# Optimization experiments

Measured on AMD Instinct MI355X. Metric: run time of the kernel, lower is better.

Reference implementation:

```python
import jax, jax.numpy as jnp
import numpy as np

B, T, D, H, L = 64, 512, 1024, 1024, 2


def _make_params(key, in_size, hidden):
    # 4 input-to-hidden and 4 hidden-to-hidden matrices, gate order (i, f, n, o),
    # concatenated along the output axis -> one GEMM per source per step.
    k1, k2 = jax.random.split(key)
    sx = (6.0 / (in_size + hidden)) ** 0.5   # xavier_uniform bound
    sh = (6.0 / (hidden + hidden)) ** 0.5
    Wx = jax.random.uniform(k1, (in_size, 4 * hidden), minval=-sx, maxval=sx, dtype=jnp.float32)
    Wh = jax.random.uniform(k2, (hidden, 4 * hidden), minval=-sh, maxval=sh, dtype=jnp.float32)
    b = jnp.zeros((4 * hidden,), dtype=jnp.float32)
    return Wx, Wh, b


def setup_inputs() -> dict:
    key = jax.random.key(0)
    kx, k0, k1 = jax.random.split(key, 3)
    x = jax.random.normal(kx, (B, T, D), dtype=jnp.float32)
    h0 = jnp.zeros((L, B, H), dtype=jnp.float32)
    c0 = jnp.zeros((L, B, H), dtype=jnp.float32)
    Wx0, Wh0, b0 = _make_params(k0, D, H)
    Wx1, Wh1, b1 = _make_params(k1, H, H)
    return {"x": x, "h0": h0, "c0": c0,
            "Wx0": Wx0, "Wh0": Wh0, "b0": b0,
            "Wx1": Wx1, "Wh1": Wh1, "b1": b1}


def _run_layer(xseq, h, c, Wx, Wh, b):
    # xseq: [T, B, in], h/c: [B, H]
    def step(carry, xt):
        h, c = carry
        g = xt @ Wx + h @ Wh + b                       # [B, 4H]
        i_t, f_t, n_t, o_t = jnp.split(g, 4, axis=-1)
        i_t = jax.nn.sigmoid(i_t)
        f_t = jax.nn.sigmoid(f_t)
        n_t = jnp.tanh(n_t)
        o_t = jax.nn.sigmoid(o_t)
        c = f_t * c + i_t * n_t
        h = o_t * jnp.tanh(c)
        return (h, c), h
    (h, c), ys = jax.lax.scan(step, (h, c), xseq)
    return ys, h, c                                     # ys: [T, B, H]


def reference(x, h0, c0, Wx0, Wh0, b0, Wx1, Wh1, b1):
    xs = jnp.transpose(x, (1, 0, 2))                    # [T, B, D]
    params = [(Wx0, Wh0, b0), (Wx1, Wh1, b1)]
    hs, cs = [], []
    for layer in range(L):
        Wx, Wh, b = params[layer]
        xs, h, c = _run_layer(xs, h0[layer], c0[layer], Wx, Wh, b)
        hs.append(h)
        cs.append(c)
    outputs = jnp.transpose(xs, (1, 0, 2))              # [B, T, H]
    return outputs, (jnp.stack(hs, 0), jnp.stack(cs, 0))
```

## Files before the change

kernel.cpp:

```cpp
#include <hip/hip_runtime.h>


#define NBLK 256
#define TPB  512
#define T_   512
#define HS_OFF 33554432
#define CS_OFF 33685504

typedef float  f32x4  __attribute__((ext_vector_type(4)));
typedef short  bf16x8 __attribute__((ext_vector_type(8)));

#define WS_CTR  0u
#define WS_W    139264u
#define WS_BIAS 33693696u
#define WS_XB   33726464u
#define WS_H0   100835328u
#define WS_H1   101097472u
#define WS_MIN  101359616u

__device__ __forceinline__ unsigned short f2bf(float f) {
  union { float f; unsigned u; } v; v.f = f;
  return (unsigned short)((v.u + 0x7FFFu + ((v.u >> 16) & 1u)) >> 16);
}
__device__ __forceinline__ float fsig(float x) { return 1.0f / (1.0f + __expf(-x)); }
__device__ __forceinline__ float ftanh(float x) {
  x = fminf(15.0f, fmaxf(-15.0f, x));
  float e = __expf(2.0f * x);
  return (e - 1.0f) / (e + 1.0f);
}

__global__ void kw(const float* __restrict__ Wx0, const float* __restrict__ Wh0,
                   const float* __restrict__ Wx1, const float* __restrict__ Wh1,
                   unsigned short* __restrict__ wp) {
  __shared__ float tile[64][65];
  int tb = blockIdx.x;
  int m  = tb >> 10;
  int kt = (tb >> 6) & 15;
  int nt = tb & 63;
  const float* W = (m == 0) ? Wx0 : (m == 1) ? Wh0 : (m == 2) ? Wx1 : Wh1;
  unsigned short* O = wp + (size_t)m * 4194304u;
  int k0 = kt * 64, n0 = nt * 64;
  int tx = threadIdx.x & 63, tg = threadIdx.x >> 6;
  for (int r = tg; r < 64; r += 4)
    tile[r][tx] = W[(size_t)(k0 + r) * 4096 + n0 + tx];
  __syncthreads();
  for (int r = tg; r < 64; r += 4) {
    int n = n0 + r;
    int p = ((n & 1023) << 2) | (n >> 10);
    O[(size_t)p * 1024 + k0 + tx] = f2bf(tile[tx][r]);
  }
}

__global__ void kx(const float* __restrict__ x, unsigned short* __restrict__ xb) {
  int row = blockIdx.x;
  int t = row >> 6, b = row & 63;
  const float4* src = (const float4*)(x + ((size_t)b * 512 + t) * 1024);
  float4 f = src[threadIdx.x];
  ushort4 o; o.x = f2bf(f.x); o.y = f2bf(f.y); o.z = f2bf(f.z); o.w = f2bf(f.w);
  ((ushort4*)(xb + (size_t)row * 1024))[threadIdx.x] = o;
}

__global__ void kmisc(const float* __restrict__ b0, const float* __restrict__ b1,
                      const float* __restrict__ h0in,
                      float* __restrict__ biasP,
                      unsigned short* __restrict__ h0r, unsigned short* __restrict__ h1r) {
  int idx = blockIdx.x * 256 + threadIdx.x;
  if (idx < 8192) {
    int layer = idx >> 12, p = idx & 4095;
    int orig = (p & 3) * 1024 + (p >> 2);
    biasP[idx] = (layer ? b1 : b0)[orig];
  } else if (idx < 139264) {
    int e = idx - 8192;
    int layer = e >> 16, o = e & 65535;
    int row = o >> 10, col = o & 1023;
    unsigned short v = f2bf(h0in[layer * 65536 + o]);
    int dst = 65536 + (col >> 3) * 512 + row * 8 + (col & 7);
    if (layer) h1r[dst] = v; else h0r[dst] = v;
  }
}

__global__ void __launch_bounds__(TPB, 2)
klstm(const float* __restrict__ c0_in,
      const unsigned short* __restrict__ wp,
      const float* __restrict__ biasP,
      const unsigned short* __restrict__ xb,
      unsigned short* __restrict__ h0ring,
      unsigned short* __restrict__ h1ring,
      unsigned* __restrict__ ctrbase,
      float* __restrict__ out) {
  extern __shared__ char smem[];
  float* red  = (float*)(smem + 131072);
  float* lhb  = (float*)(smem + 139264);
  float* xred = (float*)(smem + 141312);
  unsigned* gctr  = ctrbase;
  unsigned* rctr  = ctrbase + 16384;
  unsigned* gflag = ctrbase + 17408;
  const int tid = threadIdx.x;
  const int w   = tid >> 6;
  const int l   = tid & 63;
  const int bid = blockIdx.x;
  const int n0  = bid * 16;
  const int layer = w >> 2;
  const int rbase = (w & 3) * 16;
  const int khalf = (w >> 2) * 512;
  const int grp   = bid >> 4;
  float* lh = lhb + w * 64;

  {
    const int msrc[4] = {0, 2, 1, 3};
    for (int s = 0; s < 4; ++s) {
      const char* src = (const char*)(wp + (size_t)msrc[s] * 4194304u + (size_t)n0 * 1024u);
      char* dst = smem + s * 32768;
      for (int i = tid; i < 2048; i += TPB) {
        int kreg = i & 3, col = (i >> 2) & 15, kkf = i >> 6;
        int srcb = col * 2048 + (kkf >> 4) * 1024 + (kkf & 15) * 64 + kreg * 16;
        *(uint4*)(dst + i * 16) = *(const uint4*)(src + srcb);
      }
    }
  }

  const int jg = bid * 4 + ((l & 15) >> 2);
  const float biasv = biasP[layer * 4096 + n0 + (l & 15)];
  const int qb = l & ~3;

  float cr[4];
  #pragma unroll
  for (int v = 0; v < 4; ++v)
    cr[v] = c0_in[layer * 65536 + (rbase + (l >> 4) * 4 + v) * 1024 + jg];

  const int ae0  = (rbase + (l & 15)) * 1024 + khalf + (l >> 4) * 8;
  const int hbase = ((khalf >> 3) + (l >> 4)) * 512 + (rbase + (l & 15)) * 8;
  const int kqb   = (w >> 2) * 16384;
  const int bfrag = ((l & 15) * 4 + (l >> 4)) * 16;
  const int hsto = (bid >> 1) * 512 + 4 * (bid & 1);

  __syncthreads();

  f32x4 xacc = {0.f, 0.f, 0.f, 0.f};
  {
    #pragma unroll
    for (int kk = 0; kk < 16; ++kk) {
      bf16x8 ax = *(const bf16x8*)(xb + ae0 + kk * 32);
      bf16x8 b  = *(const bf16x8*)(smem + kqb + kk * 1024 + bfrag);
      xacc = __builtin_amdgcn_mfma_f32_16x16x32_bf16(ax, b, xacc, 0, 0, 0);
    }
    if (w >= 4) {
      float* xr = xred + (size_t)(w & 3) * 256 + (size_t)l * 4;
      #pragma unroll
      for (int v = 0; v < 4; ++v) xr[v] = xacc[v];
    }
  }
  __syncthreads();

  for (int k = 0; k <= T_; ++k) {
    const unsigned short* h0p = h0ring + ((k + 1) & 1) * 65536;
    const unsigned short* h1p = h1ring + (k & 1) * 65536;

    bf16x8 hf0[16], hf1[16];
    #pragma unroll
    for (int kk = 0; kk < 16; ++kk) {
      hf0[kk] = *(const bf16x8*)(h0p + hbase + kk * 2048);
      hf1[kk] = *(const bf16x8*)(h1p + hbase + kk * 2048);
    }

    f32x4 acc0  = {0.f, 0.f, 0.f, 0.f};
    f32x4 acc1a = {0.f, 0.f, 0.f, 0.f};
    f32x4 acc1b = {0.f, 0.f, 0.f, 0.f};
    #pragma unroll
    for (int kk = 0; kk < 16; ++kk) {
      const int bo = kqb + kk * 1024 + bfrag;
      bf16x8 bh0 = *(const bf16x8*)(smem + 65536 + bo);
      bf16x8 bx1 = *(const bf16x8*)(smem + 32768 + bo);
      bf16x8 bh1 = *(const bf16x8*)(smem + 98304 + bo);
      acc0  = __builtin_amdgcn_mfma_f32_16x16x32_bf16(hf0[kk], bh0, acc0, 0, 0, 0);
      acc1a = __builtin_amdgcn_mfma_f32_16x16x32_bf16(hf0[kk], bx1, acc1a, 0, 0, 0);
      acc1b = __builtin_amdgcn_mfma_f32_16x16x32_bf16(hf1[kk], bh1, acc1b, 0, 0, 0);
    }

    {
      float* rb = red + (size_t)(w * 64 + l) * 4;
      f32x4 other = layer ? acc0 : (acc1a + acc1b);
      #pragma unroll
      for (int v = 0; v < 4; ++v) rb[v] = other[v];
    }
    __syncthreads();

    f32x4 g = layer ? (acc1a + acc1b) : acc0;
    {
      const int pw = layer ? (w - 4) : (w + 4);
      const float* rb = red + (size_t)(pw * 64 + l) * 4;
      #pragma unroll
      for (int v = 0; v < 4; ++v) g[v] += rb[v];
    }
    if (w < 4) {
      const float* xr = xred + (size_t)w * 256 + (size_t)l * 4;
      #pragma unroll
      for (int v = 0; v < 4; ++v) g[v] += xacc[v] + xr[v];
    }

    const bool active = layer ? (k >= 1) : (k < T_);
    f32x4 outv = {0.f, 0.f, 0.f, 0.f};
    if (active) {
      unsigned short* hw = layer ? (h1ring + ((k + 1) & 1) * 65536)
                                 : (h0ring + (k & 1) * 65536);
      #pragma unroll
      for (int v = 0; v < 4; ++v) {
        float gv = g[v] + biasv;
        float gi = __shfl(gv, qb);
        float gf = __shfl(gv, qb | 1);
        float gn = __shfl(gv, qb | 2);
        float go = __shfl(gv, qb | 3);
        float i_ = fsig(gi), f_ = fsig(gf), n_ = ftanh(gn), o_ = fsig(go);
        float c = f_ * cr[v] + i_ * n_;
        cr[v] = c;
        float h = o_ * ftanh(c);
        if ((l & 3) == 0)
          lh[((l >> 4) * 4 + v) * 4 + ((l & 15) >> 2)] = h;
      }
      if (l < 16) {
        f32x4 h4 = *(f32x4*)(lh + l * 4);
        outv = h4;
        ushort4 u4;
        u4.x = f2bf(h4[0]); u4.y = f2bf(h4[1]); u4.z = f2bf(h4[2]); u4.w = f2bf(h4[3]);
        union { ushort4 s; unsigned long long q; } pk; pk.s = u4;
        __hip_atomic_store((unsigned long long*)(hw + hsto + (rbase + l) * 8), pk.q,
                           __ATOMIC_RELAXED, __HIP_MEMORY_SCOPE_AGENT);
      }
    }

    if (k < T_) {
      __syncthreads();
      if (tid == 0) {
        unsigned old = __hip_atomic_fetch_add(&gctr[grp * 1024 + k], 1u,
                                              __ATOMIC_RELAXED, __HIP_MEMORY_SCOPE_AGENT);
        if (old == 15u) {
          unsigned oldr = __hip_atomic_fetch_add(&rctr[k], 1u,
                                                 __ATOMIC_RELAXED, __HIP_MEMORY_SCOPE_AGENT);
          if (oldr == 15u) {
            #pragma unroll
            for (int gg = 0; gg < 16; ++gg)
              __hip_atomic_store(&gflag[gg * 1024 + k], 1u,
                                 __ATOMIC_RELAXED, __HIP_MEMORY_SCOPE_AGENT);
          }
        }
        __builtin_amdgcn_fence(__ATOMIC_ACQUIRE, "agent");
      }
    }

    if (active && l < 16) {
      const int row = rbase + l;
      if (layer) {
        *(f32x4*)(out + (size_t)row * 524288u + (size_t)(k - 1) * 1024u + bid * 4) = outv;
        if (k == T_)
          *(f32x4*)(out + HS_OFF + 65536 + row * 1024 + bid * 4) = outv;
      } else if (k == T_ - 1) {
        *(f32x4*)(out + HS_OFF + row * 1024 + bid * 4) = outv;
      }
    }
    if (k + 1 < T_) {
      const unsigned short* xt = xb + (size_t)(k + 1) * 65536u;
      f32x4 xa = {0.f, 0.f, 0.f, 0.f};
      #pragma unroll
      for (int kk = 0; kk < 16; ++kk) {
        bf16x8 ax = *(const bf16x8*)(xt + ae0 + kk * 32);
        bf16x8 b  = *(const bf16x8*)(smem + kqb + kk * 1024 + bfrag);
        xa = __builtin_amdgcn_mfma_f32_16x16x32_bf16(ax, b, xa, 0, 0, 0);
      }
      if (w >= 4) {
        float* xr = xred + (size_t)(w & 3) * 256 + (size_t)l * 4;
        #pragma unroll
        for (int v = 0; v < 4; ++v) xr[v] = xa[v];
      } else {
        xacc = xa;
      }
    }

    if (k < T_) {
      if (tid == 0) {
        unsigned spins = 0;
        while (__hip_atomic_load(&gflag[grp * 1024 + k], __ATOMIC_RELAXED, __HIP_MEMORY_SCOPE_AGENT) == 0u) {
          __builtin_amdgcn_s_sleep(1);
          if (++spins > 67108864u) break;
        }
      }
      __syncthreads();
    }
  }

  if ((l & 3) == 0) {
    #pragma unroll
    for (int v = 0; v < 4; ++v)
      out[CS_OFF + layer * 65536 + (rbase + (l >> 4) * 4 + v) * 1024 + jg] = cr[v];
  }
}

extern "C" void kernel_launch(void* const* d_in, const int* in_sizes, int n_in,
                              void* d_out, int out_size, void* d_ws, size_t ws_size,
                              hipStream_t stream) {
  const float* x   = (const float*)d_in[0];
  const float* h0  = (const float*)d_in[1];
  const float* c0  = (const float*)d_in[2];
  const float* Wx0 = (const float*)d_in[3];
  const float* Wh0 = (const float*)d_in[4];
  const float* b0  = (const float*)d_in[5];
  const float* Wx1 = (const float*)d_in[6];
  const float* Wh1 = (const float*)d_in[7];
  const float* b1  = (const float*)d_in[8];
  float* out = (float*)d_out;
  char* ws = (char*)d_ws;
  if (ws_size < (size_t)WS_MIN) return;

  unsigned* ctr       = (unsigned*)(ws + WS_CTR);
  unsigned short* wp  = (unsigned short*)(ws + WS_W);
  float* biasP        = (float*)(ws + WS_BIAS);
  unsigned short* xbp = (unsigned short*)(ws + WS_XB);
  unsigned short* h0r = (unsigned short*)(ws + WS_H0);
  unsigned short* h1r = (unsigned short*)(ws + WS_H1);

  (void)hipMemsetAsync(ctr, 0, 139264, stream);
  hipLaunchKernelGGL(kw,    dim3(4096),  dim3(256), 0, stream, Wx0, Wh0, Wx1, Wh1, wp);
  hipLaunchKernelGGL(kx,    dim3(32768), dim3(256), 0, stream, x, xbp);
  hipLaunchKernelGGL(kmisc, dim3(544),   dim3(256), 0, stream, b0, b1, h0, biasP, h0r, h1r);

  (void)hipFuncSetAttribute((const void*)klstm, hipFuncAttributeMaxDynamicSharedMemorySize, 145408);
  const float* c0a = c0; const unsigned short* wpa = wp; const float* bpa = biasP;
  const unsigned short* xba = xbp;
  unsigned short* h0a = h0r; unsigned short* h1a = h1r;
  unsigned* ca = ctr; float* oa = out;
  void* args[] = {&c0a, &wpa, &bpa, &xba, &h0a, &h1a, &ca, &oa};
  hipError_t e = hipLaunchCooperativeKernel((const void*)klstm, dim3(NBLK), dim3(TPB),
                                            args, 145408, stream);
  if (e != hipSuccess) {
    hipLaunchKernelGGL(klstm, dim3(NBLK), dim3(TPB), 145408, stream,
                       c0a, wpa, bpa, xba, h0a, h1a, ca, oa);
  }
}
```

Before: 5.425 ms.

## Split layers across block halves with decoupled per-layer barriers and ring buffer

Each of the 256 blocks previously computed a 16-column slice for both layers, which required an intra-block reduction and a single grid-wide barrier per step. Now blocks 0-127 handle layer 0 and blocks 128-255 handle layer 1, each block owning 32 columns with the full K range. Each layer gets its own grid counters and flags, and the layer-0 hidden state goes into an 8-deep ring so layer 0 can run up to 8 steps ahead of layer 1. The intent is to drop the cross-wave LDS reduction and let the two layers pipeline instead of running in lockstep, at the cost of more spin-wait logic and per-block work that may not balance, since layer-1 blocks perform two recurrent GEMMs per step.

```diff
diff --git a/kernel.cpp b/kernel.cpp
--- a/kernel.cpp
+++ b/kernel.cpp
@@ -11,12 +11,12 @@
 typedef short  bf16x8 __attribute__((ext_vector_type(8)));
 
 #define WS_CTR  0u
-#define WS_W    139264u
-#define WS_BIAS 33693696u
-#define WS_XB   33726464u
-#define WS_H0   100835328u
-#define WS_H1   101097472u
-#define WS_MIN  101359616u
+#define WS_W    40960u
+#define WS_BIAS 33595392u
+#define WS_XB   33628160u
+#define WS_H0   100737024u
+#define WS_H1   101785600u
+#define WS_MIN  102047744u
 
 __device__ __forceinline__ unsigned short f2bf(float f) {
   union { float f; unsigned u; } v; v.f = f;
@@ -74,8 +74,9 @@
     int layer = e >> 16, o = e & 65535;
     int row = o >> 10, col = o & 1023;
     unsigned short v = f2bf(h0in[layer * 65536 + o]);
-    int dst = 65536 + (col >> 3) * 512 + row * 8 + (col & 7);
-    if (layer) h1r[dst] = v; else h0r[dst] = v;
+    int ds = (col >> 3) * 512 + row * 8 + (col & 7);
+    if (layer) h1r[65536 + ds] = v;
+    else       h0r[7 * 65536 + ds] = v;
   }
 }
 
@@ -89,120 +90,132 @@
       unsigned* __restrict__ ctrbase,
       float* __restrict__ out) {
   extern __shared__ char smem[];
-  float* red  = (float*)(smem + 131072);
-  float* lhb  = (float*)(smem + 139264);
-  float* xred = (float*)(smem + 141312);
-  unsigned* gctr  = ctrbase;
-  unsigned* rctr  = ctrbase + 16384;
-  unsigned* gflag = ctrbase + 17408;
+  float* lhb = (float*)(smem + 131072);
+  unsigned* gctr0 = ctrbase;
+  unsigned* rctr0 = ctrbase + 4096;
+  unsigned* flag0 = ctrbase + 4608;
+  unsigned* gctr1 = ctrbase + 5120;
+  unsigned* rctr1 = ctrbase + 9216;
+  unsigned* flag1 = ctrbase + 9728;
   const int tid = threadIdx.x;
   const int w   = tid >> 6;
   const int l   = tid & 63;
   const int bid = blockIdx.x;
-  const int n0  = bid * 16;
-  const int layer = w >> 2;
+  const int isL1 = bid >> 7;
+  const int b    = bid & 127;
+  const int cg   = w >> 2;
   const int rbase = (w & 3) * 16;
-  const int khalf = (w >> 2) * 512;
-  const int grp   = bid >> 4;
+  const int n0   = b * 32;
+  const int grp  = b >> 4;
   float* lh = lhb + w * 64;
 
   {
-    const int msrc[4] = {0, 2, 1, 3};
-    for (int s = 0; s < 4; ++s) {
-      const char* src = (const char*)(wp + (size_t)msrc[s] * 4194304u + (size_t)n0 * 1024u);
-      char* dst = smem + s * 32768;
-      for (int i = tid; i < 2048; i += TPB) {
-        int kreg = i & 3, col = (i >> 2) & 15, kkf = i >> 6;
-        int srcb = col * 2048 + (kkf >> 4) * 1024 + (kkf & 15) * 64 + kreg * 16;
+    const int mA = isL1 ? 3 : 1;
+    const int mB = isL1 ? 2 : 0;
+    for (int s = 0; s < 2; ++s) {
+      int m = s ? mB : mA;
+      const char* src = (const char*)(wp + (size_t)m * 4194304u + (size_t)n0 * 1024u);
+      char* dst = smem + s * 65536;
+      for (int i = tid; i < 4096; i += TPB) {
+        int kreg = i & 3, col = (i >> 2) & 15, kk = (i >> 6) & 31, cgg = i >> 11;
+        int srcb = (cgg * 16 + col) * 2048 + kk * 64 + kreg * 16;
         *(uint4*)(dst + i * 16) = *(const uint4*)(src + srcb);
       }
     }
   }
 
-  const int jg = bid * 4 + ((l & 15) >> 2);
-  const float biasv = biasP[layer * 4096 + n0 + (l & 15)];
+  const float biasv = biasP[isL1 * 4096 + n0 + cg * 16 + (l & 15)];
   const int qb = l & ~3;
+  const int jg = b * 8 + cg * 4 + ((l & 15) >> 2);
 
   float cr[4];
   #pragma unroll
   for (int v = 0; v < 4; ++v)
-    cr[v] = c0_in[layer * 65536 + (rbase + (l >> 4) * 4 + v) * 1024 + jg];
-
-  const int ae0  = (rbase + (l & 15)) * 1024 + khalf + (l >> 4) * 8;
-  const int hbase = ((khalf >> 3) + (l >> 4)) * 512 + (rbase + (l & 15)) * 8;
-  const int kqb   = (w >> 2) * 16384;
+    cr[v] = c0_in[isL1 * 65536 + (rbase + (l >> 4) * 4 + v) * 1024 + jg];
+
+  const int hfb   = (l >> 4) * 512 + (rbase + (l & 15)) * 8;
   const int bfrag = ((l & 15) * 4 + (l >> 4)) * 16;
-  const int hsto = (bid >> 1) * 512 + 4 * (bid & 1);
+  const int ae0   = (rbase + (l & 15)) * 1024 + (l >> 4) * 8;
+  const int bslot0 = cg * 32768;
+  const int bslot1 = 65536 + cg * 32768;
+  const int hsto  = b * 512 + cg * 4;
 
   __syncthreads();
 
   f32x4 xacc = {0.f, 0.f, 0.f, 0.f};
-  {
+  if (!isL1) {
     #pragma unroll
-    for (int kk = 0; kk < 16; ++kk) {
+    for (int kk = 0; kk < 32; ++kk) {
       bf16x8 ax = *(const bf16x8*)(xb + ae0 + kk * 32);
-      bf16x8 b  = *(const bf16x8*)(smem + kqb + kk * 1024 + bfrag);
-      xacc = __builtin_amdgcn_mfma_f32_16x16x32_bf16(ax, b, xacc, 0, 0, 0);
-    }
-    if (w >= 4) {
-      float* xr = xred + (size_t)(w & 3) * 256 + (size_t)l * 4;
-      #pragma unroll
-      for (int v = 0; v < 4; ++v) xr[v] = xacc[v];
-    }
-  }
-  __syncthreads();
-
-  for (int k = 0; k <= T_; ++k) {
-    const unsigned short* h0p = h0ring + ((k + 1) & 1) * 65536;
-    const unsigned short* h1p = h1ring + (k & 1) * 65536;
-
-    bf16x8 hf0[16], hf1[16];
-    #pragma unroll
-    for (int kk = 0; kk < 16; ++kk) {
-      hf0[kk] = *(const bf16x8*)(h0p + hbase + kk * 2048);
-      hf1[kk] = *(const bf16x8*)(h1p + hbase + kk * 2048);
-    }
-
-    f32x4 acc0  = {0.f, 0.f, 0.f, 0.f};
-    f32x4 acc1a = {0.f, 0.f, 0.f, 0.f};
-    f32x4 acc1b = {0.f, 0.f, 0.f, 0.f};
-    #pragma unroll
-    for (int kk = 0; kk < 16; ++kk) {
-      const int bo = kqb + kk * 1024 + bfrag;
-      bf16x8 bh0 = *(const bf16x8*)(smem + 65536 + bo);
-      bf16x8 bx1 = *(const bf16x8*)(smem + 32768 + bo);
-      bf16x8 bh1 = *(const bf16x8*)(smem + 98304 + bo);
-      acc0  = __builtin_amdgcn_mfma_f32_16x16x32_bf16(hf0[kk], bh0, acc0, 0, 0, 0);
-      acc1a = __builtin_amdgcn_mfma_f32_16x16x32_bf16(hf0[kk], bx1, acc1a, 0, 0, 0);
-      acc1b = __builtin_amdgcn_mfma_f32_16x16x32_bf16(hf1[kk], bh1, acc1b, 0, 0, 0);
-    }
-
+      bf16x8 bx = *(const bf16x8*)(smem + bslot1 + kk * 1024 + bfrag);
+      xacc = __builtin_amdgcn_mfma_f32_16x16x32_bf16(ax, bx, xacc, 0, 0, 0);
+    }
+  }
+
+  for (int k = 0; k < T_; ++k) {
+    if (tid == 0) {
+      unsigned spins = 0;
+      if (!isL1) {
+        if (k > 0)
+          while (__hip_atomic_load(&flag0[k - 1], __ATOMIC_RELAXED, __HIP_MEMORY_SCOPE_AGENT) == 0u)
+            { __builtin_amdgcn_s_sleep(1); if (++spins > 67108864u) break; }
+        if (k >= 8)
+          while (__hip_atomic_load(&flag1[k - 8], __ATOMIC_RELAXED, __HIP_MEMORY_SCOPE_AGENT) == 0u)
+            { __builtin_amdgcn_s_sleep(1); if (++spins > 67108864u) break; }
+      } else {
+        if (k > 0)
+          while (__hip_atomic_load(&flag1[k - 1], __ATOMIC_RELAXED, __HIP_MEMORY_SCOPE_AGENT) == 0u)
+            { __builtin_amdgcn_s_sleep(1); if (++spins > 67108864u) break; }
+        while (__hip_atomic_load(&flag0[k], __ATOMIC_RELAXED, __HIP_MEMORY_SCOPE_AGENT) == 0u)
+          { __builtin_amdgcn_s_sleep(1); if (++spins > 67108864u) break; }
+      }
+    }
+    __syncthreads();
+
+    f32x4 a0 = {0.f,0.f,0.f,0.f}, a1 = {0.f,0.f,0.f,0.f};
+    f32x4 a2 = {0.f,0.f,0.f,0.f}, a3 = {0.f,0.f,0.f,0.f};
+    if (!isL1) {
+      const unsigned short* hp = h0ring + (size_t)((k + 7) & 7) * 65536;
+      bf16x8 hf[32];
+      #pragma unroll
+      for (int kk = 0; kk < 32; ++kk) hf[kk] = *(const bf16x8*)(hp + hfb + kk * 2048);
+      #pragma unroll
+      for (int kk = 0; kk < 32; kk += 2) {
+        a0 = __builtin_amdgcn_mfma_f32_16x16x32_bf16(hf[kk],
+               *(const bf16x8*)(smem + bslot0 + kk * 1024 + bfrag), a0, 0, 0, 0);
+        a1 = __builtin_amdgcn_mfma_f32_16x16x32_bf16(hf[kk + 1],
+               *(const bf16x8*)(smem + bslot0 + (kk + 1) * 1024 + bfrag), a1, 0, 0, 0);
+      }
+    } else {
+      const unsigned short* hp0 = h0ring + (size_t)(k & 7) * 65536;
+      const unsigned short* hp1 = h1ring + (size_t)((k + 1) & 1) * 65536;
+      #pragma unroll
+      for (int kk = 0; kk < 32; kk += 2) {
+        bf16x8 f0a = *(const bf16x8*)(hp0 + hfb + kk * 2048);
+        bf16x8 f1a = *(const bf16x8*)(hp1 + hfb + kk * 2048);
+        bf16x8 f0b = *(const bf16x8*)(hp0 + hfb + (kk + 1) * 2048);
+        bf16x8 f1b = *(const bf16x8*)(hp1 + hfb + (kk + 1) * 2048);
+        a0 = __builtin_amdgcn_mfma_f32_16x16x32_bf16(f1a,
+               *(const bf16x8*)(smem + bslot0 + kk * 1024 + bfrag), a0, 0, 0, 0);
+        a2 = __builtin_amdgcn_mfma_f32_16x16x32_bf16(f0a,
+               *(const bf16x8*)(smem + bslot1 + kk * 1024 + bfrag), a2, 0, 0, 0);
+        a1 = __builtin_amdgcn_mfma_f32_16x16x32_bf16(f1b,
+               *(const bf16x8*)(smem + bslot0 + (kk + 1) * 1024 + bfrag), a1, 0, 0, 0);
+        a3 = __builtin_amdgcn_mfma_f32_16x16x32_bf16(f0b,
+               *(const bf16x8*)(smem + bslot1 + (kk + 1) * 1024 + bfrag), a3, 0, 0, 0);
+      }
+    }
+
+    f32x4 g = (a0 + a1) + (a2 + a3);
+    if (!isL1) {
+      #pragma unroll
+      for (int v = 0; v < 4; ++v) g[v] += xacc[v];
+    }
+
+    f32x4 outv = {0.f, 0.f, 0.f, 0.f};
     {
-      float* rb = red + (size_t)(w * 64 + l) * 4;
-      f32x4 other = layer ? acc0 : (acc1a + acc1b);
-      #pragma unroll
-      for (int v = 0; v < 4; ++v) rb[v] = other[v];
-    }
-    __syncthreads();
-
-    f32x4 g = layer ? (acc1a + acc1b) : acc0;
-    {
-      const int pw = layer ? (w - 4) : (w + 4);
-      const float* rb = red + (size_t)(pw * 64 + l) * 4;
-      #pragma unroll
-      for (int v = 0; v < 4; ++v) g[v] += rb[v];
-    }
-    if (w < 4) {
-      const float* xr = xred + (size_t)w * 256 + (size_t)l * 4;
-      #pragma unroll
-      for (int v = 0; v < 4; ++v) g[v] += xacc[v] + xr[v];
-    }
-
-    const bool active = layer ? (k >= 1) : (k < T_);
-    f32x4 outv = {0.f, 0.f, 0.f, 0.f};
-    if (active) {
-      unsigned short* hw = layer ? (h1ring + ((k + 1) & 1) * 65536)
-                                 : (h0ring + (k & 1) * 65536);
+      unsigned short* hw = isL1 ? (h1ring + (size_t)(k & 1) * 65536)
+                                : (h0ring + (size_t)(k & 7) * 65536);
       #pragma unroll
       for (int v = 0; v < 4; ++v) {
         float gv = g[v] + biasv;
@@ -228,69 +241,48 @@
       }
     }
 
-    if (k < T_) {
-      __syncthreads();
-      if (tid == 0) {
-        unsigned old = __hip_atomic_fetch_add(&gctr[grp * 1024 + k], 1u,
-                                              __ATOMIC_RELAXED, __HIP_MEMORY_SCOPE_AGENT);
-        if (old == 15u) {
-          unsigned oldr = __hip_atomic_fetch_add(&rctr[k], 1u,
-                                                 __ATOMIC_RELAXED, __HIP_MEMORY_SCOPE_AGENT);
-          if (oldr == 15u) {
-            #pragma unroll
-            for (int gg = 0; gg < 16; ++gg)
-              __hip_atomic_store(&gflag[gg * 1024 + k], 1u,
-                                 __ATOMIC_RELAXED, __HIP_MEMORY_SCOPE_AGENT);
-          }
+    __syncthreads();
+    if (tid == 0) {
+      unsigned* gc = (isL1 ? gctr1 : gctr0) + grp * 512 + k;
+      unsigned old = __hip_atomic_fetch_add(gc, 1u, __ATOMIC_RELAXED, __HIP_MEMORY_SCOPE_AGENT);
+      if (old == 15u) {
+        unsigned* rc = (isL1 ? rctr1 : rctr0) + k;
+        unsigned oldr = __hip_atomic_fetch_add(rc, 1u, __ATOMIC_RELAXED, __HIP_MEMORY_SCOPE_AGENT);
+        if (oldr == 7u)
+          __hip_atomic_store(&(isL1 ? flag1 : flag0)[k], 1u,
+                             __ATOMIC_RELAXED, __HIP_MEMORY_SCOPE_AGENT);
+      }
+      __builtin_amdgcn_fence(__ATOMIC_ACQUIRE, "agent");
+    }
+
+    if (isL1) {
+      if (l < 16) {
+        const int row = rbase + l;
+        *(f32x4*)(out + (size_t)row * 524288u + (size_t)k * 1024u + b * 8 + cg * 4) = outv;
+        if (k == T_ - 1)
+          *(f32x4*)(out + HS_OFF + 65536 + row * 1024 + b * 8 + cg * 4) = outv;
+      }
+    } else {
+      if (k == T_ - 1 && l < 16)
+        *(f32x4*)(out + HS_OFF + (rbase + l) * 1024 + b * 8 + cg * 4) = outv;
+      if (k + 1 < T_) {
+        const unsigned short* xt = xb + (size_t)(k + 1) * 65536u;
+        f32x4 xa = {0.f, 0.f, 0.f, 0.f};
+        #pragma unroll
+        for (int kk = 0; kk < 32; ++kk) {
+          bf16x8 ax = *(const bf16x8*)(xt + ae0 + kk * 32);
+          bf16x8 bx = *(const bf16x8*)(smem + bslot1 + kk * 1024 + bfrag);
+          xa = __builtin_amdgcn_mfma_f32_16x16x32_bf16(ax, bx, xa, 0, 0, 0);
         }
-        __builtin_amdgcn_fence(__ATOMIC_ACQUIRE, "agent");
-      }
-    }
-
-    if (active && l < 16) {
-      const int row = rbase + l;
-      if (layer) {
-        *(f32x4*)(out + (size_t)row * 524288u + (size_t)(k - 1) * 1024u + bid * 4) = outv;
-        if (k == T_)
-          *(f32x4*)(out + HS_OFF + 65536 + row * 1024 + bid * 4) = outv;
-      } else if (k == T_ - 1) {
-        *(f32x4*)(out + HS_OFF + row * 1024 + bid * 4) = outv;
-      }
-    }
-    if (k + 1 < T_) {
-      const unsigned short* xt = xb + (size_t)(k + 1) * 65536u;
-      f32x4 xa = {0.f, 0.f, 0.f, 0.f};
-      #pragma unroll
-      for (int kk = 0; kk < 16; ++kk) {
-        bf16x8 ax = *(const bf16x8*)(xt + ae0 + kk * 32);
-        bf16x8 b  = *(const bf16x8*)(smem + kqb + kk * 1024 + bfrag);
-        xa = __builtin_amdgcn_mfma_f32_16x16x32_bf16(ax, b, xa, 0, 0, 0);
-      }
-      if (w >= 4) {
-        float* xr = xred + (size_t)(w & 3) * 256 + (size_t)l * 4;
-        #pragma unroll
-        for (int v = 0; v < 4; ++v) xr[v] = xa[v];
-      } else {
         xacc = xa;
       }
-    }
-
-    if (k < T_) {
-      if (tid == 0) {
-        unsigned spins = 0;
-        while (__hip_atomic_load(&gflag[grp * 1024 + k], __ATOMIC_RELAXED, __HIP_MEMORY_SCOPE_AGENT) == 0u) {
-          __builtin_amdgcn_s_sleep(1);
-          if (++spins > 67108864u) break;
-        }
-      }
-      __syncthreads();
     }
   }
 
   if ((l & 3) == 0) {
     #pragma unroll
     for (int v = 0; v < 4; ++v)
-      out[CS_OFF + layer * 65536 + (rbase + (l >> 4) * 4 + v) * 1024 + jg] = cr[v];
+      out[CS_OFF + isL1 * 65536 + (rbase + (l >> 4) * 4 + v) * 1024 + jg] = cr[v];
   }
 }
 
@@ -317,21 +309,21 @@
   unsigned short* h0r = (unsigned short*)(ws + WS_H0);
   unsigned short* h1r = (unsigned short*)(ws + WS_H1);
 
-  (void)hipMemsetAsync(ctr, 0, 139264, stream);
+  (void)hipMemsetAsync(ctr, 0, 40960, stream);
   hipLaunchKernelGGL(kw,    dim3(4096),  dim3(256), 0, stream, Wx0, Wh0, Wx1, Wh1, wp);
   hipLaunchKernelGGL(kx,    dim3(32768), dim3(256), 0, stream, x, xbp);
   hipLaunchKernelGGL(kmisc, dim3(544),   dim3(256), 0, stream, b0, b1, h0, biasP, h0r, h1r);
 
-  (void)hipFuncSetAttribute((const void*)klstm, hipFuncAttributeMaxDynamicSharedMemorySize, 145408);
+  (void)hipFuncSetAttribute((const void*)klstm, hipFuncAttributeMaxDynamicSharedMemorySize, 133120);
   const float* c0a = c0; const unsigned short* wpa = wp; const float* bpa = biasP;
   const unsigned short* xba = xbp;
   unsigned short* h0a = h0r; unsigned short* h1a = h1r;
   unsigned* ca = ctr; float* oa = out;
   void* args[] = {&c0a, &wpa, &bpa, &xba, &h0a, &h1a, &ca, &oa};
   hipError_t e = hipLaunchCooperativeKernel((const void*)klstm, dim3(NBLK), dim3(TPB),
-                                            args, 145408, stream);
+                                            args, 133120, stream);
   if (e != hipSuccess) {
-    hipLaunchKernelGGL(klstm, dim3(NBLK), dim3(TPB), 145408, stream,
+    hipLaunchKernelGGL(klstm, dim3(NBLK), dim3(TPB), 133120, stream,
                        c0a, wpa, bpa, xba, h0a, h1a, ca, oa);
   }
 }
```

New measurement: 6.197 ms. +14.2%, slower.
